# Kernel tuning notes

Measured on AMD Instinct MI355X. Metric: run time of the kernel, lower is better.

The kernel has to match this reference:

```python
import jax, jax.numpy as jnp
import numpy as np

N_NODES = 50000
N_EDGES = 500000
D = 128
H = 128


def setup_inputs() -> dict:
    key = jax.random.key(0)
    ks = jax.random.split(key, 10)
    s = lambda fan_in: 1.0 / np.sqrt(fan_in)
    return {
        "nodes": jax.random.normal(ks[0], (N_NODES, D), jnp.float32),
        "edges": jax.random.normal(ks[1], (N_EDGES, D), jnp.float32),
        "receivers": jax.random.randint(ks[2], (N_EDGES,), 0, N_NODES, jnp.int32),
        "senders": jax.random.randint(ks[3], (N_EDGES,), 0, N_NODES, jnp.int32),
        "global_latent": jax.random.normal(ks[4], (1, D), jnp.float32),
        "eW1": jax.random.normal(ks[5], (3 * D, H), jnp.float32) * s(3 * D),
        "eb1": jnp.zeros((H,), jnp.float32),
        "eW2": jax.random.normal(ks[6], (H, D), jnp.float32) * s(H),
        "eb2": jnp.zeros((D,), jnp.float32),
        "nW1": jax.random.normal(ks[7], (2 * D, H), jnp.float32) * s(2 * D),
        "nb1": jnp.zeros((H,), jnp.float32),
        "nW2": jax.random.normal(ks[8], (H, D), jnp.float32) * s(H),
        "nb2": jnp.zeros((D,), jnp.float32),
        "rm_w": jnp.full((1,), -5.0, jnp.float32),  # softplus resnet multiplier init
    }


def reference(nodes, edges, receivers, senders, global_latent,
              eW1, eb1, eW2, eb2, nW1, nb1, nW2, nb2, rm_w):
    # gather node attributes at edge endpoints
    received = jnp.take(nodes, receivers, axis=0)   # [E, D]
    sent = jnp.take(nodes, senders, axis=0)         # [E, D]
    # edge model: concat + 2-layer MLP (relu)
    e_in = jnp.concatenate([edges, sent, received], axis=1)   # [E, 3D]
    e_upd = jax.nn.relu(e_in @ eW1 + eb1) @ eW2 + eb2          # [E, D]
    # scatter-sum messages to receiver nodes
    adjacent = jax.ops.segment_sum(e_upd, receivers, num_segments=nodes.shape[0])  # [N, D]
    # node model: concat + 2-layer MLP (relu)
    n_in = jnp.concatenate([nodes, adjacent], axis=1)          # [N, 2D]
    n_upd = jax.nn.relu(n_in @ nW1 + nb1) @ nW2 + nb2          # [N, D]
    # residual with softplus multiplier (dropout inactive in eval)
    mult = jax.nn.softplus(rm_w)
    edges_out = edges + mult * e_upd
    nodes_out = nodes + mult * n_upd
    return (nodes_out, edges_out)
```

## Files before the change

### kernel.cpp

```cpp
#include <hip/hip_runtime.h>
#include <hip/hip_bf16.h>

#define NN 50000
#define NE 500000

typedef __attribute__((ext_vector_type(4))) float f32x4;
typedef __attribute__((ext_vector_type(8))) short bf16x8;
typedef unsigned short u16;

#define LDK 136
#define LDK2 264

#define MFMA16(a, b, c) __builtin_amdgcn_mfma_f32_16x16x32_bf16((a), (b), (c), 0, 0, 0)

__device__ __forceinline__ float bf2f(u16 u) {
    union { unsigned int i; float f; } v; v.i = ((unsigned int)u) << 16; return v.f;
}
__device__ __forceinline__ u16 f2bf(float f) {
    union { float f; unsigned int i; } v; v.f = f;
    return (u16)((v.i + 0x7fffu + ((v.i >> 16) & 1u)) >> 16);
}

__global__ void prep_w(const float* __restrict__ eW1, const float* __restrict__ eW2,
                       const float* __restrict__ nW1, const float* __restrict__ nW2,
                       u16* __restrict__ W1at, u16* __restrict__ eW2t, u16* __restrict__ Wbct,
                       u16* __restrict__ nW1t, u16* __restrict__ nW2t) {
    int idx = blockIdx.x * blockDim.x + threadIdx.x;
    if (idx < 16384) { int j = idx >> 7, k = idx & 127; W1at[j * 128 + k] = f2bf(eW1[k * 128 + j]); return; }
    idx -= 16384;
    if (idx < 16384) { int j = idx >> 7, k = idx & 127; eW2t[j * 128 + k] = f2bf(eW2[k * 128 + j]); return; }
    idx -= 16384;
    if (idx < 32768) {
        int j = idx >> 7, k = idx & 127;
        float v = (j < 128) ? eW1[(128 + k) * 128 + j] : eW1[(256 + k) * 128 + (j - 128)];
        Wbct[j * 128 + k] = f2bf(v); return;
    }
    idx -= 32768;
    if (idx < 32768) { int j = idx >> 8, k = idx & 255; nW1t[j * 256 + k] = f2bf(nW1[k * 128 + j]); return; }
    idx -= 32768;
    if (idx < 16384) { int j = idx >> 7, k = idx & 127; nW2t[j * 128 + k] = f2bf(nW2[k * 128 + j]); return; }
}

__global__ __launch_bounds__(512)
void node_pq(const float* __restrict__ nodes, const u16* __restrict__ Wbct,
             u16* __restrict__ PQw) {
    __shared__ u16 Xs[64 * LDK];
    __shared__ u16 Ws[256 * LDK];
    const int tid = threadIdx.x;
    const int n0 = blockIdx.x * 64;
    const int nvalid = min(64, NN - n0);

    for (int idx = tid; idx < 64 * 32; idx += 512) {
        int row = idx >> 5, c4 = idx & 31;
        int nd = n0 + row; if (nd >= NN) nd = NN - 1;
        float4 v = *(const float4*)(nodes + (size_t)nd * 128 + c4 * 4);
        ushort4 u; u.x = f2bf(v.x); u.y = f2bf(v.y); u.z = f2bf(v.z); u.w = f2bf(v.w);
        *(ushort4*)(Xs + row * LDK + c4 * 4) = u;
    }
    for (int idx = tid; idx < 256 * 16; idx += 512) {
        int row = idx >> 4, c = idx & 15;
        *(int4*)(Ws + row * LDK + c * 8) = *(const int4*)(Wbct + row * 128 + c * 8);
    }
    __syncthreads();

    const int lane = tid & 63;
    const int w = tid >> 6;
    const int cb = w * 32;
    const int l15 = lane & 15, l4 = lane >> 4;

    f32x4 acc[4][2] = {};
#pragma unroll
    for (int k0 = 0; k0 < 128; k0 += 32) {
        bf16x8 a[4], b[2];
#pragma unroll
        for (int f = 0; f < 4; ++f)
            a[f] = *(const bf16x8*)(Xs + (f * 16 + l15) * LDK + k0 + l4 * 8);
#pragma unroll
        for (int f = 0; f < 2; ++f)
            b[f] = *(const bf16x8*)(Ws + (cb + f * 16 + l15) * LDK + k0 + l4 * 8);
#pragma unroll
        for (int i = 0; i < 4; ++i)
#pragma unroll
            for (int j = 0; j < 2; ++j)
                acc[i][j] = MFMA16(a[i], b[j], acc[i][j]);
    }
#pragma unroll
    for (int i = 0; i < 4; ++i)
#pragma unroll
        for (int j = 0; j < 2; ++j) {
            int n = cb + j * 16 + l15;
#pragma unroll
            for (int v = 0; v < 4; ++v) {
                int m = i * 16 + l4 * 4 + v;
                if (m < nvalid) PQw[(size_t)(n0 + m) * 256 + n] = f2bf(acc[i][j][v]);
            }
        }
}

__global__ __launch_bounds__(512)
void edge_mlp(const float* __restrict__ edges,
              const int* __restrict__ recv, const int* __restrict__ send,
              const u16* __restrict__ PQw,
              const u16* __restrict__ W1at, const u16* __restrict__ W2t,
              const float* __restrict__ eb1, const float* __restrict__ eb2,
              const float* __restrict__ rm_w,
              float* __restrict__ edges_out, float* __restrict__ adj) {
    __shared__ u16 Xs[64 * LDK];
    __shared__ u16 PQs[64 * LDK2];
    __shared__ u16 W1s[128 * LDK];
    __shared__ u16 W2s[128 * LDK];
    __shared__ u16 Hs[64 * LDK];
    __shared__ int Rs[64];

    const int tid = threadIdx.x;
    const int e0 = blockIdx.x * 64;
    const int nvalid = min(64, NE - e0);
    const float mult = log1pf(expf(rm_w[0]));

    for (int idx = tid; idx < 64 * 32; idx += 512) {
        int row = idx >> 5, c4 = idx & 31;
        int e = e0 + row; if (e >= NE) e = NE - 1;
        float4 v = *(const float4*)(edges + (size_t)e * 128 + c4 * 4);
        ushort4 u; u.x = f2bf(v.x); u.y = f2bf(v.y); u.z = f2bf(v.z); u.w = f2bf(v.w);
        *(ushort4*)(Xs + row * LDK + c4 * 4) = u;
    }
    if (tid < 64) {
        int e = e0 + tid; if (e >= NE) e = NE - 1;
        Rs[tid] = recv[e];
    }
    for (int idx = tid; idx < 64 * 32; idx += 512) {
        int row = idx >> 5, half = (idx >> 4) & 1, c = idx & 15;
        int e = e0 + row; if (e >= NE) e = NE - 1;
        int node = half ? recv[e] : send[e];
        int4 v = *(const int4*)(PQw + (size_t)node * 256 + half * 128 + c * 8);
        *(int4*)(PQs + row * LDK2 + half * 128 + c * 8) = v;
    }
    for (int idx = tid; idx < 128 * 16; idx += 512) {
        int row = idx >> 4, c = idx & 15;
        *(int4*)(W1s + row * LDK + c * 8) = *(const int4*)(W1at + row * 128 + c * 8);
        *(int4*)(W2s + row * LDK + c * 8) = *(const int4*)(W2t + row * 128 + c * 8);
    }
    __syncthreads();

    const int lane = tid & 63;
    const int w = tid >> 6;
    const int rb = (w >> 2) * 32, cb = (w & 3) * 32;
    const int l15 = lane & 15, l4 = lane >> 4;

    f32x4 acc[2][2] = {};
#pragma unroll
    for (int k0 = 0; k0 < 128; k0 += 32) {
        bf16x8 a[2], b[2];
#pragma unroll
        for (int f = 0; f < 2; ++f) {
            a[f] = *(const bf16x8*)(Xs + (rb + f * 16 + l15) * LDK + k0 + l4 * 8);
            b[f] = *(const bf16x8*)(W1s + (cb + f * 16 + l15) * LDK + k0 + l4 * 8);
        }
#pragma unroll
        for (int i = 0; i < 2; ++i)
#pragma unroll
            for (int j = 0; j < 2; ++j)
                acc[i][j] = MFMA16(a[i], b[j], acc[i][j]);
    }

#pragma unroll
    for (int i = 0; i < 2; ++i)
#pragma unroll
        for (int j = 0; j < 2; ++j) {
            int n = cb + j * 16 + l15;
            float b1 = eb1[n];
#pragma unroll
            for (int v = 0; v < 4; ++v) {
                int m = rb + i * 16 + l4 * 4 + v;
                float val = acc[i][j][v] + b1
                          + bf2f(PQs[m * LDK2 + n]) + bf2f(PQs[m * LDK2 + 128 + n]);
                Hs[m * LDK + n] = f2bf(fmaxf(val, 0.f));
            }
        }
    __syncthreads();

    f32x4 acc2[2][2] = {};
#pragma unroll
    for (int k0 = 0; k0 < 128; k0 += 32) {
        bf16x8 a[2], b[2];
#pragma unroll
        for (int f = 0; f < 2; ++f) {
            a[f] = *(const bf16x8*)(Hs + (rb + f * 16 + l15) * LDK + k0 + l4 * 8);
            b[f] = *(const bf16x8*)(W2s + (cb + f * 16 + l15) * LDK + k0 + l4 * 8);
        }
#pragma unroll
        for (int i = 0; i < 2; ++i)
#pragma unroll
            for (int j = 0; j < 2; ++j)
                acc2[i][j] = MFMA16(a[i], b[j], acc2[i][j]);
    }

#pragma unroll
    for (int i = 0; i < 2; ++i)
#pragma unroll
        for (int j = 0; j < 2; ++j) {
            int n = cb + j * 16 + l15;
            float b2 = eb2[n];
#pragma unroll
            for (int v = 0; v < 4; ++v) {
                int m = rb + i * 16 + l4 * 4 + v;
                if (m < nvalid) {
                    float upd = acc2[i][j][v] + b2;
                    size_t off = (size_t)(e0 + m) * 128 + n;
                    edges_out[off] = edges[off] + mult * upd;
                    unsafeAtomicAdd(adj + (size_t)Rs[m] * 128 + n, upd);
                }
            }
        }
}

__global__ __launch_bounds__(512)
void node_mlp(const float* __restrict__ nodes, const float* __restrict__ adj,
              const u16* __restrict__ W1t,
              const u16* __restrict__ W2t,
              const float* __restrict__ nb1, const float* __restrict__ nb2,
              const float* __restrict__ rm_w, float* __restrict__ nodes_out) {
    __shared__ u16 Xs[64 * LDK2];
    __shared__ u16 W1s[128 * LDK2];
    __shared__ u16 W2s[128 * LDK];
    __shared__ u16 Hs[64 * LDK];

    const int tid = threadIdx.x;
    const int n0 = blockIdx.x * 64;
    const int nvalid = min(64, NN - n0);
    const float mult = log1pf(expf(rm_w[0]));

    for (int idx = tid; idx < 64 * 64; idx += 512) {
        int row = idx >> 6, c4 = idx & 63;
        int nd = n0 + row; if (nd >= NN) nd = NN - 1;
        const float* src = (c4 < 32) ? (nodes + (size_t)nd * 128 + c4 * 4)
                                     : (adj + (size_t)nd * 128 + (c4 - 32) * 4);
        float4 v = *(const float4*)src;
        ushort4 u; u.x = f2bf(v.x); u.y = f2bf(v.y); u.z = f2bf(v.z); u.w = f2bf(v.w);
        *(ushort4*)(Xs + row * LDK2 + c4 * 4) = u;
    }
    for (int idx = tid; idx < 128 * 32; idx += 512) {
        int row = idx >> 5, c = idx & 31;
        *(int4*)(W1s + row * LDK2 + c * 8) = *(const int4*)(W1t + row * 256 + c * 8);
    }
    for (int idx = tid; idx < 128 * 16; idx += 512) {
        int row = idx >> 4, c = idx & 15;
        *(int4*)(W2s + row * LDK + c * 8) = *(const int4*)(W2t + row * 128 + c * 8);
    }
    __syncthreads();

    const int lane = tid & 63;
    const int w = tid >> 6;
    const int rb = (w >> 2) * 32, cb = (w & 3) * 32;
    const int l15 = lane & 15, l4 = lane >> 4;

    f32x4 acc[2][2] = {};
#pragma unroll
    for (int k0 = 0; k0 < 256; k0 += 32) {
        bf16x8 a[2], b[2];
#pragma unroll
        for (int f = 0; f < 2; ++f) {
            a[f] = *(const bf16x8*)(Xs + (rb + f * 16 + l15) * LDK2 + k0 + l4 * 8);
            b[f] = *(const bf16x8*)(W1s + (cb + f * 16 + l15) * LDK2 + k0 + l4 * 8);
        }
#pragma unroll
        for (int i = 0; i < 2; ++i)
#pragma unroll
            for (int j = 0; j < 2; ++j)
                acc[i][j] = MFMA16(a[i], b[j], acc[i][j]);
    }

#pragma unroll
    for (int i = 0; i < 2; ++i)
#pragma unroll
        for (int j = 0; j < 2; ++j) {
            int n = cb + j * 16 + l15;
            float b1 = nb1[n];
#pragma unroll
            for (int v = 0; v < 4; ++v) {
                int m = rb + i * 16 + l4 * 4 + v;
                Hs[m * LDK + n] = f2bf(fmaxf(acc[i][j][v] + b1, 0.f));
            }
        }
    __syncthreads();

    f32x4 acc2[2][2] = {};
#pragma unroll
    for (int k0 = 0; k0 < 128; k0 += 32) {
        bf16x8 a[2], b[2];
#pragma unroll
        for (int f = 0; f < 2; ++f) {
            a[f] = *(const bf16x8*)(Hs + (rb + f * 16 + l15) * LDK + k0 + l4 * 8);
            b[f] = *(const bf16x8*)(W2s + (cb + f * 16 + l15) * LDK + k0 + l4 * 8);
        }
#pragma unroll
        for (int i = 0; i < 2; ++i)
#pragma unroll
            for (int j = 0; j < 2; ++j)
                acc2[i][j] = MFMA16(a[i], b[j], acc2[i][j]);
    }

#pragma unroll
    for (int i = 0; i < 2; ++i)
#pragma unroll
        for (int j = 0; j < 2; ++j) {
            int n = cb + j * 16 + l15;
            float b2 = nb2[n];
#pragma unroll
            for (int v = 0; v < 4; ++v) {
                int m = rb + i * 16 + l4 * 4 + v;
                if (m < nvalid) {
                    size_t off = (size_t)(n0 + m) * 128 + n;
                    nodes_out[off] = nodes[off] + mult * (acc2[i][j][v] + b2);
                }
            }
        }
}

extern "C" void kernel_launch(void* const* d_in, const int* in_sizes, int n_in,
                              void* d_out, int out_size, void* d_ws, size_t ws_size,
                              hipStream_t stream) {
    const float* nodes     = (const float*)d_in[0];
    const float* edges     = (const float*)d_in[1];
    const int*   receivers = (const int*)d_in[2];
    const int*   senders   = (const int*)d_in[3];
    const float* eW1  = (const float*)d_in[5];
    const float* eb1  = (const float*)d_in[6];
    const float* eW2  = (const float*)d_in[7];
    const float* eb2  = (const float*)d_in[8];
    const float* nW1  = (const float*)d_in[9];
    const float* nb1  = (const float*)d_in[10];
    const float* nW2  = (const float*)d_in[11];
    const float* nb2  = (const float*)d_in[12];
    const float* rm_w = (const float*)d_in[13];

    char* ws = (char*)d_ws;
    u16*   PQw  = (u16*)(ws + 0);
    float* adj  = (float*)(ws + 25600000);
    u16*   W1at = (u16*)(ws + 51200000);
    u16*   eW2t = (u16*)(ws + 51232768);
    u16*   Wbct = (u16*)(ws + 51265536);
    u16*   nW1t = (u16*)(ws + 51331072);
    u16*   nW2t = (u16*)(ws + 51396608);

    float* nodes_out = (float*)d_out;
    float* edges_out = (float*)d_out + (size_t)NN * 128;

    hipMemsetAsync(adj, 0, (size_t)NN * 128 * sizeof(float), stream);
    prep_w<<<448, 256, 0, stream>>>(eW1, eW2, nW1, nW2, W1at, eW2t, Wbct, nW1t, nW2t);
    node_pq<<<(NN + 63) / 64, 512, 0, stream>>>(nodes, Wbct, PQw);
    edge_mlp<<<(NE + 63) / 64, 512, 0, stream>>>(edges, receivers, senders, PQw, W1at, eW2t,
                                                 eb1, eb2, rm_w, edges_out, adj);
    node_mlp<<<(NN + 63) / 64, 512, 0, stream>>>(nodes, adj, nW1t, nW2t, nb1, nb2, rm_w,
                                                 nodes_out);
}
```

Baseline: 918.0 us.

## Hold weight fragments in registers instead of staging weights through LDS

```diff
diff --git a/kernel.cpp b/kernel.cpp
--- a/kernel.cpp
+++ b/kernel.cpp
@@ -41,14 +41,24 @@
     if (idx < 16384) { int j = idx >> 7, k = idx & 127; nW2t[j * 128 + k] = f2bf(nW2[k * 128 + j]); return; }
 }
 
-__global__ __launch_bounds__(512)
+__global__ __launch_bounds__(512, 4)
 void node_pq(const float* __restrict__ nodes, const u16* __restrict__ Wbct,
              u16* __restrict__ PQw) {
     __shared__ u16 Xs[64 * LDK];
-    __shared__ u16 Ws[256 * LDK];
     const int tid = threadIdx.x;
+    const int lane = tid & 63;
+    const int w = tid >> 6;
+    const int l15 = lane & 15, l4 = lane >> 4;
+    const int cb = w * 32;
     const int n0 = blockIdx.x * 64;
     const int nvalid = min(64, NN - n0);
+
+    bf16x8 bw[2][4];
+#pragma unroll
+    for (int kk = 0; kk < 4; ++kk)
+#pragma unroll
+        for (int j = 0; j < 2; ++j)
+            bw[j][kk] = *(const bf16x8*)(Wbct + (cb + j * 16 + l15) * 128 + kk * 32 + l4 * 8);
 
     for (int idx = tid; idx < 64 * 32; idx += 512) {
         int row = idx >> 5, c4 = idx & 31;
@@ -57,32 +67,18 @@
         ushort4 u; u.x = f2bf(v.x); u.y = f2bf(v.y); u.z = f2bf(v.z); u.w = f2bf(v.w);
         *(ushort4*)(Xs + row * LDK + c4 * 4) = u;
     }
-    for (int idx = tid; idx < 256 * 16; idx += 512) {
-        int row = idx >> 4, c = idx & 15;
-        *(int4*)(Ws + row * LDK + c * 8) = *(const int4*)(Wbct + row * 128 + c * 8);
-    }
-    __syncthreads();
-
-    const int lane = tid & 63;
-    const int w = tid >> 6;
-    const int cb = w * 32;
-    const int l15 = lane & 15, l4 = lane >> 4;
+    __syncthreads();
 
     f32x4 acc[4][2] = {};
 #pragma unroll
-    for (int k0 = 0; k0 < 128; k0 += 32) {
-        bf16x8 a[4], b[2];
-#pragma unroll
-        for (int f = 0; f < 4; ++f)
-            a[f] = *(const bf16x8*)(Xs + (f * 16 + l15) * LDK + k0 + l4 * 8);
-#pragma unroll
-        for (int f = 0; f < 2; ++f)
-            b[f] = *(const bf16x8*)(Ws + (cb + f * 16 + l15) * LDK + k0 + l4 * 8);
-#pragma unroll
-        for (int i = 0; i < 4; ++i)
+    for (int kk = 0; kk < 4; ++kk) {
+#pragma unroll
+        for (int f = 0; f < 4; ++f) {
+            bf16x8 a = *(const bf16x8*)(Xs + (f * 16 + l15) * LDK + kk * 32 + l4 * 8);
 #pragma unroll
             for (int j = 0; j < 2; ++j)
-                acc[i][j] = MFMA16(a[i], b[j], acc[i][j]);
+                acc[f][j] = MFMA16(a, bw[j][kk], acc[f][j]);
+        }
     }
 #pragma unroll
     for (int i = 0; i < 4; ++i)
@@ -97,7 +93,7 @@
         }
 }
 
-__global__ __launch_bounds__(512)
+__global__ __launch_bounds__(512, 4)
 void edge_mlp(const float* __restrict__ edges,
               const int* __restrict__ recv, const int* __restrict__ send,
               const u16* __restrict__ PQw,
@@ -107,15 +103,24 @@
               float* __restrict__ edges_out, float* __restrict__ adj) {
     __shared__ u16 Xs[64 * LDK];
     __shared__ u16 PQs[64 * LDK2];
-    __shared__ u16 W1s[128 * LDK];
-    __shared__ u16 W2s[128 * LDK];
     __shared__ u16 Hs[64 * LDK];
     __shared__ int Rs[64];
 
     const int tid = threadIdx.x;
+    const int lane = tid & 63;
+    const int w = tid >> 6;
+    const int l15 = lane & 15, l4 = lane >> 4;
+    const int cb = w * 16;
     const int e0 = blockIdx.x * 64;
     const int nvalid = min(64, NE - e0);
     const float mult = log1pf(expf(rm_w[0]));
+
+    bf16x8 bw1[4], bw2[4];
+#pragma unroll
+    for (int kk = 0; kk < 4; ++kk) {
+        bw1[kk] = *(const bf16x8*)(W1at + (cb + l15) * 128 + kk * 32 + l4 * 8);
+        bw2[kk] = *(const bf16x8*)(W2t + (cb + l15) * 128 + kk * 32 + l4 * 8);
+    }
 
     for (int idx = tid; idx < 64 * 32; idx += 512) {
         int row = idx >> 5, c4 = idx & 31;
@@ -135,100 +140,86 @@
         int4 v = *(const int4*)(PQw + (size_t)node * 256 + half * 128 + c * 8);
         *(int4*)(PQs + row * LDK2 + half * 128 + c * 8) = v;
     }
-    for (int idx = tid; idx < 128 * 16; idx += 512) {
-        int row = idx >> 4, c = idx & 15;
-        *(int4*)(W1s + row * LDK + c * 8) = *(const int4*)(W1at + row * 128 + c * 8);
-        *(int4*)(W2s + row * LDK + c * 8) = *(const int4*)(W2t + row * 128 + c * 8);
-    }
-    __syncthreads();
-
-    const int lane = tid & 63;
-    const int w = tid >> 6;
-    const int rb = (w >> 2) * 32, cb = (w & 3) * 32;
-    const int l15 = lane & 15, l4 = lane >> 4;
-
-    f32x4 acc[2][2] = {};
-#pragma unroll
-    for (int k0 = 0; k0 < 128; k0 += 32) {
-        bf16x8 a[2], b[2];
-#pragma unroll
-        for (int f = 0; f < 2; ++f) {
-            a[f] = *(const bf16x8*)(Xs + (rb + f * 16 + l15) * LDK + k0 + l4 * 8);
-            b[f] = *(const bf16x8*)(W1s + (cb + f * 16 + l15) * LDK + k0 + l4 * 8);
-        }
-#pragma unroll
-        for (int i = 0; i < 2; ++i)
-#pragma unroll
-            for (int j = 0; j < 2; ++j)
-                acc[i][j] = MFMA16(a[i], b[j], acc[i][j]);
-    }
-
-#pragma unroll
-    for (int i = 0; i < 2; ++i)
-#pragma unroll
-        for (int j = 0; j < 2; ++j) {
-            int n = cb + j * 16 + l15;
-            float b1 = eb1[n];
-#pragma unroll
-            for (int v = 0; v < 4; ++v) {
-                int m = rb + i * 16 + l4 * 4 + v;
-                float val = acc[i][j][v] + b1
+    __syncthreads();
+
+    f32x4 acc[4] = {};
+#pragma unroll
+    for (int kk = 0; kk < 4; ++kk) {
+#pragma unroll
+        for (int f = 0; f < 4; ++f) {
+            bf16x8 a = *(const bf16x8*)(Xs + (f * 16 + l15) * LDK + kk * 32 + l4 * 8);
+            acc[f] = MFMA16(a, bw1[kk], acc[f]);
+        }
+    }
+
+    {
+        const int n = cb + l15;
+        const float b1 = eb1[n];
+#pragma unroll
+        for (int i = 0; i < 4; ++i)
+#pragma unroll
+            for (int v = 0; v < 4; ++v) {
+                int m = i * 16 + l4 * 4 + v;
+                float val = acc[i][v] + b1
                           + bf2f(PQs[m * LDK2 + n]) + bf2f(PQs[m * LDK2 + 128 + n]);
                 Hs[m * LDK + n] = f2bf(fmaxf(val, 0.f));
             }
-        }
-    __syncthreads();
-
-    f32x4 acc2[2][2] = {};
-#pragma unroll
-    for (int k0 = 0; k0 < 128; k0 += 32) {
-        bf16x8 a[2], b[2];
-#pragma unroll
-        for (int f = 0; f < 2; ++f) {
-            a[f] = *(const bf16x8*)(Hs + (rb + f * 16 + l15) * LDK + k0 + l4 * 8);
-            b[f] = *(const bf16x8*)(W2s + (cb + f * 16 + l15) * LDK + k0 + l4 * 8);
-        }
-#pragma unroll
-        for (int i = 0; i < 2; ++i)
-#pragma unroll
-            for (int j = 0; j < 2; ++j)
-                acc2[i][j] = MFMA16(a[i], b[j], acc2[i][j]);
-    }
-
-#pragma unroll
-    for (int i = 0; i < 2; ++i)
-#pragma unroll
-        for (int j = 0; j < 2; ++j) {
-            int n = cb + j * 16 + l15;
-            float b2 = eb2[n];
-#pragma unroll
-            for (int v = 0; v < 4; ++v) {
-                int m = rb + i * 16 + l4 * 4 + v;
+    }
+    __syncthreads();
+
+    f32x4 acc2[4] = {};
+#pragma unroll
+    for (int kk = 0; kk < 4; ++kk) {
+#pragma unroll
+        for (int f = 0; f < 4; ++f) {
+            bf16x8 a = *(const bf16x8*)(Hs + (f * 16 + l15) * LDK + kk * 32 + l4 * 8);
+            acc2[f] = MFMA16(a, bw2[kk], acc2[f]);
+        }
+    }
+
+    {
+        const int n = cb + l15;
+        const float b2 = eb2[n];
+#pragma unroll
+        for (int i = 0; i < 4; ++i)
+#pragma unroll
+            for (int v = 0; v < 4; ++v) {
+                int m = i * 16 + l4 * 4 + v;
                 if (m < nvalid) {
-                    float upd = acc2[i][j][v] + b2;
+                    float upd = acc2[i][v] + b2;
                     size_t off = (size_t)(e0 + m) * 128 + n;
                     edges_out[off] = edges[off] + mult * upd;
                     unsafeAtomicAdd(adj + (size_t)Rs[m] * 128 + n, upd);
                 }
             }
-        }
-}
-
-__global__ __launch_bounds__(512)
+    }
+}
+
+__global__ __launch_bounds__(512, 4)
 void node_mlp(const float* __restrict__ nodes, const float* __restrict__ adj,
               const u16* __restrict__ W1t,
               const u16* __restrict__ W2t,
               const float* __restrict__ nb1, const float* __restrict__ nb2,
               const float* __restrict__ rm_w, float* __restrict__ nodes_out) {
     __shared__ u16 Xs[64 * LDK2];
-    __shared__ u16 W1s[128 * LDK2];
-    __shared__ u16 W2s[128 * LDK];
     __shared__ u16 Hs[64 * LDK];
 
     const int tid = threadIdx.x;
+    const int lane = tid & 63;
+    const int w = tid >> 6;
+    const int l15 = lane & 15, l4 = lane >> 4;
+    const int cb = w * 16;
     const int n0 = blockIdx.x * 64;
     const int nvalid = min(64, NN - n0);
     const float mult = log1pf(expf(rm_w[0]));
+
+    bf16x8 bw1[8], bw2[4];
+#pragma unroll
+    for (int kk = 0; kk < 8; ++kk)
+        bw1[kk] = *(const bf16x8*)(W1t + (cb + l15) * 256 + kk * 32 + l4 * 8);
+#pragma unroll
+    for (int kk = 0; kk < 4; ++kk)
+        bw2[kk] = *(const bf16x8*)(W2t + (cb + l15) * 128 + kk * 32 + l4 * 8);
 
     for (int idx = tid; idx < 64 * 64; idx += 512) {
         int row = idx >> 6, c4 = idx & 63;
@@ -239,82 +230,55 @@
         ushort4 u; u.x = f2bf(v.x); u.y = f2bf(v.y); u.z = f2bf(v.z); u.w = f2bf(v.w);
         *(ushort4*)(Xs + row * LDK2 + c4 * 4) = u;
     }
-    for (int idx = tid; idx < 128 * 32; idx += 512) {
-        int row = idx >> 5, c = idx & 31;
-        *(int4*)(W1s + row * LDK2 + c * 8) = *(const int4*)(W1t + row * 256 + c * 8);
-    }
-    for (int idx = tid; idx < 128 * 16; idx += 512) {
-        int row = idx >> 4, c = idx & 15;
-        *(int4*)(W2s + row * LDK + c * 8) = *(const int4*)(W2t + row * 128 + c * 8);
-    }
-    __syncthreads();
-
-    const int lane = tid & 63;
-    const int w = tid >> 6;
-    const int rb = (w >> 2) * 32, cb = (w & 3) * 32;
-    const int l15 = lane & 15, l4 = lane >> 4;
-
-    f32x4 acc[2][2] = {};
-#pragma unroll
-    for (int k0 = 0; k0 < 256; k0 += 32) {
-        bf16x8 a[2], b[2];
-#pragma unroll
-        for (int f = 0; f < 2; ++f) {
-            a[f] = *(const bf16x8*)(Xs + (rb + f * 16 + l15) * LDK2 + k0 + l4 * 8);
-            b[f] = *(const bf16x8*)(W1s + (cb + f * 16 + l15) * LDK2 + k0 + l4 * 8);
-        }
-#pragma unroll
-        for (int i = 0; i < 2; ++i)
-#pragma unroll
-            for (int j = 0; j < 2; ++j)
-                acc[i][j] = MFMA16(a[i], b[j], acc[i][j]);
-    }
-
-#pragma unroll
-    for (int i = 0; i < 2; ++i)
-#pragma unroll
-        for (int j = 0; j < 2; ++j) {
-            int n = cb + j * 16 + l15;
-            float b1 = nb1[n];
-#pragma unroll
-            for (int v = 0; v < 4; ++v) {
-                int m = rb + i * 16 + l4 * 4 + v;
-                Hs[m * LDK + n] = f2bf(fmaxf(acc[i][j][v] + b1, 0.f));
-            }
-        }
-    __syncthreads();
-
-    f32x4 acc2[2][2] = {};
-#pragma unroll
-    for (int k0 = 0; k0 < 128; k0 += 32) {
-        bf16x8 a[2], b[2];
-#pragma unroll
-        for (int f = 0; f < 2; ++f) {
-            a[f] = *(const bf16x8*)(Hs + (rb + f * 16 + l15) * LDK + k0 + l4 * 8);
-            b[f] = *(const bf16x8*)(W2s + (cb + f * 16 + l15) * LDK + k0 + l4 * 8);
-        }
-#pragma unroll
-        for (int i = 0; i < 2; ++i)
-#pragma unroll
-            for (int j = 0; j < 2; ++j)
-                acc2[i][j] = MFMA16(a[i], b[j], acc2[i][j]);
-    }
-
-#pragma unroll
-    for (int i = 0; i < 2; ++i)
-#pragma unroll
-        for (int j = 0; j < 2; ++j) {
-            int n = cb + j * 16 + l15;
-            float b2 = nb2[n];
-#pragma unroll
-            for (int v = 0; v < 4; ++v) {
-                int m = rb + i * 16 + l4 * 4 + v;
+    __syncthreads();
+
+    f32x4 acc[4] = {};
+#pragma unroll
+    for (int kk = 0; kk < 8; ++kk) {
+#pragma unroll
+        for (int f = 0; f < 4; ++f) {
+            bf16x8 a = *(const bf16x8*)(Xs + (f * 16 + l15) * LDK2 + kk * 32 + l4 * 8);
+            acc[f] = MFMA16(a, bw1[kk], acc[f]);
+        }
+    }
+
+    {
+        const int n = cb + l15;
+        const float b1 = nb1[n];
+#pragma unroll
+        for (int i = 0; i < 4; ++i)
+#pragma unroll
+            for (int v = 0; v < 4; ++v) {
+                int m = i * 16 + l4 * 4 + v;
+                Hs[m * LDK + n] = f2bf(fmaxf(acc[i][v] + b1, 0.f));
+            }
+    }
+    __syncthreads();
+
+    f32x4 acc2[4] = {};
+#pragma unroll
+    for (int kk = 0; kk < 4; ++kk) {
+#pragma unroll
+        for (int f = 0; f < 4; ++f) {
+            bf16x8 a = *(const bf16x8*)(Hs + (f * 16 + l15) * LDK + kk * 32 + l4 * 8);
+            acc2[f] = MFMA16(a, bw2[kk], acc2[f]);
+        }
+    }
+
+    {
+        const int n = cb + l15;
+        const float b2 = nb2[n];
+#pragma unroll
+        for (int i = 0; i < 4; ++i)
+#pragma unroll
+            for (int v = 0; v < 4; ++v) {
+                int m = i * 16 + l4 * 4 + v;
                 if (m < nvalid) {
                     size_t off = (size_t)(n0 + m) * 128 + n;
-                    nodes_out[off] = nodes[off] + mult * (acc2[i][j][v] + b2);
+                    nodes_out[off] = nodes[off] + mult * (acc2[i][v] + b2);
                 }
             }
-        }
+    }
 }
 
 extern "C" void kernel_launch(void* const* d_in, const int* in_sizes, int n_in,
```

Result: faster. 784.9 us (-14.5%).
